# Optimization experiments

Measured on AMD Instinct MI355X. Metric: run time of the kernel, lower is better.

Reference implementation:

```python
import jax, jax.numpy as jnp
import numpy as np

N_NODES = 50000
N_EDGES = 800000
IN_FEATS = 256
H_FEATS = 256
NUM_CLASSES = 16
NUM_GRAPHS = 64


def _glorot(key, shape):
    lim = float(np.sqrt(6.0 / (shape[0] + shape[1])))
    return jax.random.uniform(key, shape, jnp.float32, -lim, lim)


def setup_inputs() -> dict:
    key = jax.random.key(0)
    ks = jax.random.split(key, 12)
    x = jax.random.normal(ks[0], (N_NODES, IN_FEATS), jnp.float32)
    edge_index = jax.random.randint(ks[1], (2, N_EDGES), 0, N_NODES, jnp.int64)
    batch_vec = jnp.sort(jax.random.randint(ks[2], (N_NODES,), 0, NUM_GRAPHS, jnp.int64))
    W1 = _glorot(ks[3], (IN_FEATS, H_FEATS)); b1 = jnp.zeros((H_FEATS,), jnp.float32)
    W2 = _glorot(ks[4], (H_FEATS, H_FEATS)); b2 = jnp.zeros((H_FEATS,), jnp.float32)
    W3 = _glorot(ks[5], (H_FEATS, H_FEATS)); b3 = jnp.zeros((H_FEATS,), jnp.float32)
    W4 = _glorot(ks[6], (H_FEATS, NUM_CLASSES)); b4 = jnp.zeros((NUM_CLASSES,), jnp.float32)
    return {"x": x, "edge_index": edge_index, "batch_vec": batch_vec,
            "W1": W1, "b1": b1, "W2": W2, "b2": b2,
            "W3": W3, "b3": b3, "W4": W4, "b4": b4}


def gcn_conv(x, W, b, src, dst, deg_inv_sqrt):
    # PyG GCNConv: out = D^{-1/2} (A + I) D^{-1/2} (x W) + b
    h = x @ W  # [N, F_out]
    norm = deg_inv_sqrt[src] * deg_inv_sqrt[dst]  # [E+N]
    msgs = h[src] * norm[:, None]  # gather + scale
    agg = jax.ops.segment_sum(msgs, dst, num_segments=x.shape[0])
    return agg + b


def reference(x, edge_index, batch_vec, W1, b1, W2, b2, W3, b3, W4, b4):
    n = x.shape[0]
    # add self-loops once (shared across layers)
    loops = jnp.arange(n, dtype=edge_index.dtype)
    src = jnp.concatenate([edge_index[0], loops])
    dst = jnp.concatenate([edge_index[1], loops])
    deg = jax.ops.segment_sum(jnp.ones_like(dst, dtype=x.dtype), dst, num_segments=n)
    deg_inv_sqrt = jnp.where(deg > 0, jax.lax.rsqrt(deg), 0.0)

    h = gcn_conv(x, W1, b1, src, dst, deg_inv_sqrt)
    h_copy = jax.nn.relu(h)
    # dropout is identity in eval mode (training=False)
    h = gcn_conv(h_copy, W2, b2, src, dst, deg_inv_sqrt)
    h_copy = jax.nn.relu(jax.nn.relu(h) + h_copy)
    h = gcn_conv(h_copy, W3, b3, src, dst, deg_inv_sqrt)
    h = jax.nn.relu(jax.nn.relu(h) + h_copy)
    h = gcn_conv(h, W4, b4, src, dst, deg_inv_sqrt)

    # global_mean_pool over batch vector
    sums = jax.ops.segment_sum(h, batch_vec, num_segments=NUM_GRAPHS)
    counts = jax.ops.segment_sum(jnp.ones((n,), h.dtype), batch_vec, num_segments=NUM_GRAPHS)
    return sums / jnp.maximum(counts, 1.0)[:, None]
```

## Files before the change

### kernel.cpp

```cpp
#include <hip/hip_runtime.h>
#include <hip/hip_bf16.h>

#define N_NODES 50000
#define N_EDGES 800000
#define F 256
#define NGRAPH 64
#define NCLS 16
#define NBLK_N 196

typedef short short8 __attribute__((ext_vector_type(8)));
typedef float f32x4 __attribute__((ext_vector_type(4)));

__device__ __forceinline__ float bf2f(ushort u) {
    unsigned v = ((unsigned)u) << 16;
    return __uint_as_float(v);
}
__device__ __forceinline__ ushort f2bf(float f) {
    __hip_bfloat16 b = __float2bfloat16(f);
    return *reinterpret_cast<ushort*>(&b);
}
__device__ __forceinline__ float bflo(uint u) { return __uint_as_float(u << 16); }
__device__ __forceinline__ float bfhi(uint u) { return __uint_as_float(u & 0xffff0000u); }


__global__ __launch_bounds__(256) void k_init(int* __restrict__ ecnt,
                                              float* __restrict__ pool,
                                              float* __restrict__ cnt) {
    int i = blockIdx.x * 256 + threadIdx.x;
    if (i < N_NODES) ecnt[i] = 0;
    if (i < NGRAPH * NCLS) pool[i] = 0.f;
    if (i < NGRAPH) cnt[i] = 0.f;
}

__global__ __launch_bounds__(256) void k_count(const int* __restrict__ dst,
                                               int* __restrict__ ecnt) {
    int e = blockIdx.x * 256 + threadIdx.x;
    if (e < N_EDGES) atomicAdd(&ecnt[dst[e]], 1);
}

__global__ __launch_bounds__(256) void k_scan_block(const int* __restrict__ ecnt,
                                                    int* __restrict__ rowptr,
                                                    int* __restrict__ blkSum,
                                                    float* __restrict__ dinv,
                                                    float* __restrict__ sdeg) {
    __shared__ int sh[256];
    int i = blockIdx.x * 256 + threadIdx.x;
    int v = (i < N_NODES) ? ecnt[i] : 0;
    sh[threadIdx.x] = v;
    __syncthreads();
#pragma unroll
    for (int off = 1; off < 256; off <<= 1) {
        int t = (threadIdx.x >= off) ? sh[threadIdx.x - off] : 0;
        __syncthreads();
        sh[threadIdx.x] += t;
        __syncthreads();
    }
    if (i < N_NODES) {
        rowptr[i] = sh[threadIdx.x] - v;
        float d = (float)(v + 1);
        dinv[i] = rsqrtf(d);
        sdeg[i] = sqrtf(d);
    }
    if (threadIdx.x == 255) blkSum[blockIdx.x] = sh[255];
}

__global__ __launch_bounds__(256) void k_scan_add(const int* __restrict__ blkSum,
                                                  int* __restrict__ rowptr,
                                                  int* __restrict__ cursor) {
    __shared__ int sh[256];
    int t = threadIdx.x;
    sh[t] = (t < NBLK_N && t < (int)blockIdx.x) ? blkSum[t] : 0;
    __syncthreads();
#pragma unroll
    for (int off = 128; off > 0; off >>= 1) {
        if (t < off) sh[t] += sh[t + off];
        __syncthreads();
    }
    int base = sh[0];
    int i = blockIdx.x * 256 + t;
    if (i < N_NODES) {
        int r = rowptr[i] + base;
        rowptr[i] = r;
        cursor[i] = r;
    }
    if (i == 0) rowptr[N_NODES] = N_EDGES;
}

__global__ __launch_bounds__(256) void k_fill_csr(const int* __restrict__ src,
                                                  const int* __restrict__ dst,
                                                  int* __restrict__ cursor,
                                                  ushort* __restrict__ csr16) {
    int e = blockIdx.x * 256 + threadIdx.x;
    if (e >= N_EDGES) return;
    int s = src[e];
    int d = dst[e];
    int p = atomicAdd(&cursor[d], 1);
    csr16[p] = (ushort)s;
}


__global__ __launch_bounds__(256) void k_prescale(const float* __restrict__ x,
                                                  const float* __restrict__ dinv,
                                                  ushort* __restrict__ T0) {
    int i = blockIdx.x * 256 + threadIdx.x;
    if (i >= (int)((size_t)N_NODES * F / 8)) return;
    int n = i >> 5;
    float di = dinv[n];
    const float4* ip = (const float4*)(x + (size_t)i * 8);
    float4 a = ip[0], b = ip[1];
    short8 v;
    v[0] = (short)f2bf(a.x * di); v[1] = (short)f2bf(a.y * di);
    v[2] = (short)f2bf(a.z * di); v[3] = (short)f2bf(a.w * di);
    v[4] = (short)f2bf(b.x * di); v[5] = (short)f2bf(b.y * di);
    v[6] = (short)f2bf(b.z * di); v[7] = (short)f2bf(b.w * di);
    *(short8*)(T0 + (size_t)i * 8) = v;
}


__global__ __launch_bounds__(256) void k_wpack(const float* __restrict__ W1,
                                               const float* __restrict__ W2,
                                               const float* __restrict__ W3,
                                               const float* __restrict__ W4,
                                               ushort* __restrict__ Wp,
                                               ushort* __restrict__ Wp4) {
    int gid = blockIdx.x * 256 + threadIdx.x;
    if (gid < 24576) {
        int which = gid >> 13;
        int idx = gid & 8191;
        const float* W = (which == 0) ? W1 : (which == 1) ? W2 : W3;
        ushort* o = Wp + (size_t)which * 65536;
        int lane = idx & 63;
        int ks = (idx >> 6) & 7;
        int ctg = idx >> 9;
        int kbase = ks * 32 + (lane >> 4) * 8;
        int col = ctg * 16 + (lane & 15);
        short8 v;
#pragma unroll
        for (int e = 0; e < 8; ++e)
            v[e] = (short)f2bf(W[(size_t)(kbase + e) * 256 + col]);
        *(short8*)(o + (size_t)idx * 8) = v;
    } else if (gid < 24576 + 512) {
        int idx = gid - 24576;
        int lane = idx & 63;
        int ks = idx >> 6;
        int kbase = ks * 32 + (lane >> 4) * 8;
        int col = lane & 15;
        short8 v;
#pragma unroll
        for (int e = 0; e < 8; ++e)
            v[e] = (short)f2bf(W4[(size_t)(kbase + e) * 16 + col]);
        *(short8*)(Wp4 + (size_t)idx * 8) = v;
    }
}


template <int MODE>
__global__ __launch_bounds__(256) void k_layer(const ushort* __restrict__ Hs,
                                               const ushort* __restrict__ Wp,
                                               const float* __restrict__ bias,
                                               const float* __restrict__ dinv,
                                               const float* __restrict__ sdeg,
                                               const int* __restrict__ rowptr,
                                               const ushort* __restrict__ csr16,
                                               ushort* __restrict__ OUT,
                                               const ushort* __restrict__ Wp4,
                                               ushort* __restrict__ G16) {
    __shared__ __align__(16) ushort At[16 * 264];
    __shared__ __align__(16) ushort cs[4][16 * 72];
    const int t = threadIdx.x;
    const int wv = t >> 6;
    const int l = t & 63;
    const int m0 = blockIdx.x * 16;

    {
        const int slot = l >> 5;
        const int c = (l & 31) * 8;
#pragma unroll
        for (int rep = 0; rep < 4; ++rep) {
            const int noderow = wv * 4 + rep;
            const int n = m0 + noderow;
            const bool valid = n < N_NODES;
            const int nn = valid ? n : 0;

            float acc[8];
#pragma unroll
            for (int j = 0; j < 8; ++j) acc[j] = 0.f;

            int i = valid ? rowptr[nn] + slot : 0;
            const int end = valid ? rowptr[nn + 1] : 0;
            for (; i + 6 < end; i += 8) {
                int s0 = csr16[i], s1 = csr16[i + 2], s2 = csr16[i + 4], s3 = csr16[i + 6];
                short8 v0 = *(const short8*)(Hs + (size_t)s0 * F + c);
                short8 v1 = *(const short8*)(Hs + (size_t)s1 * F + c);
                short8 v2 = *(const short8*)(Hs + (size_t)s2 * F + c);
                short8 v3 = *(const short8*)(Hs + (size_t)s3 * F + c);
#pragma unroll
                for (int j = 0; j < 8; ++j)
                    acc[j] += (bf2f((ushort)v0[j]) + bf2f((ushort)v1[j])) +
                              (bf2f((ushort)v2[j]) + bf2f((ushort)v3[j]));
            }
            for (; i < end; i += 2) {
                int s0 = csr16[i];
                short8 v0 = *(const short8*)(Hs + (size_t)s0 * F + c);
#pragma unroll
                for (int j = 0; j < 8; ++j) acc[j] += bf2f((ushort)v0[j]);
            }

#pragma unroll
            for (int j = 0; j < 8; ++j) acc[j] += __shfl_xor(acc[j], 32);

            if (slot == 0) {
                short8 av;
                if (valid) {
                    const short8 h = *(const short8*)(Hs + (size_t)nn * F + c);
                    float di = dinv[nn];
#pragma unroll
                    for (int j = 0; j < 8; ++j)
                        av[j] = (short)f2bf(di * (acc[j] + bf2f((ushort)h[j])));
                } else {
#pragma unroll
                    for (int j = 0; j < 8; ++j) av[j] = 0;
                }
                *(short8*)&At[noderow * 264 + c] = av;
            }
        }
    }
    __syncthreads();

    const int colbase = wv * 64;
    const int lrow = l & 15;
    const int lk = (l >> 4) * 8;
    const short8* wp = (const short8*)Wp;

    short8 af[8];
#pragma unroll
    for (int ks = 0; ks < 8; ++ks)
        af[ks] = *(const short8*)&At[lrow * 264 + lk + ks * 32];

#pragma unroll
    for (int ct = 0; ct < 4; ++ct) {
        short8 wf[8];
#pragma unroll
        for (int ks = 0; ks < 8; ++ks)
            wf[ks] = wp[(size_t)(((wv * 4 + ct) * 8 + ks) * 64) + l];

        f32x4 acc = (f32x4){0.f, 0.f, 0.f, 0.f};
#pragma unroll
        for (int ks = 0; ks < 8; ++ks)
            acc = __builtin_amdgcn_mfma_f32_16x16x32_bf16(af[ks], wf[ks], acc, 0, 0, 0);

        int col = ct * 16 + (l & 15);
#pragma unroll
        for (int r = 0; r < 4; ++r) {
            int row = (l >> 4) * 4 + r;
            cs[wv][row * 72 + col] = f2bf(acc[r]);
        }
    }
#pragma unroll
    for (int h = 0; h < 2; ++h) {
        int row = h * 8 + (l >> 3);
        int coff = (l & 7) * 8;
        int orow = m0 + row;
        if (orow < N_NODES) {
            short8 z8 = *(const short8*)&cs[wv][row * 72 + coff];
            int gcol = colbase + coff;
            const float4 b0 = *(const float4*)(bias + gcol);
            const float4 b1 = *(const float4*)(bias + gcol + 4);
            float bb[8] = {b0.x, b0.y, b0.z, b0.w, b1.x, b1.y, b1.z, b1.w};
            float di = dinv[orow];
            short8 ov;
            if (MODE >= 2) {
                const short8 hp = *(const short8*)(Hs + (size_t)orow * F + gcol);
                float sd = sdeg[orow];
#pragma unroll
                for (int j = 0; j < 8; ++j) {
                    float u = fmaxf(bf2f((ushort)z8[j]) + bb[j], 0.f);
                    u = fmaxf(u + bf2f((ushort)hp[j]) * sd, 0.f);
                    ov[j] = (short)f2bf(u * di);
                }
            } else {
#pragma unroll
                for (int j = 0; j < 8; ++j) {
                    float u = fmaxf(bf2f((ushort)z8[j]) + bb[j], 0.f);
                    ov[j] = (short)f2bf(u * di);
                }
            }
            if (MODE == 3) {
                *(short8*)&cs[wv][row * 72 + coff] = ov;
            } else {
                *(short8*)(OUT + (size_t)orow * F + gcol) = ov;
            }
        } else if (MODE == 3) {
            short8 zv;
#pragma unroll
            for (int j = 0; j < 8; ++j) zv[j] = 0;
            *(short8*)&cs[wv][row * 72 + coff] = zv;
        }
    }

    if (MODE == 3) {
        __syncthreads();
        if (wv == 0) {
            const short8* wp4 = (const short8*)Wp4;
            f32x4 acc = (f32x4){0.f, 0.f, 0.f, 0.f};
#pragma unroll
            for (int ks = 0; ks < 8; ++ks) {
                int cbase = lk + ks * 32;
                short8 a2 = *(const short8*)&cs[cbase >> 6][lrow * 72 + (cbase & 63)];
                short8 w4 = wp4[(size_t)(ks * 64) + l];
                acc = __builtin_amdgcn_mfma_f32_16x16x32_bf16(a2, w4, acc, 0, 0, 0);
            }
            int col = l & 15;
#pragma unroll
            for (int r = 0; r < 4; ++r) {
                int row = (l >> 4) * 4 + r;
                int orow = m0 + row;
                if (orow < N_NODES)
                    G16[(size_t)orow * 16 + col] = f2bf(acc[r]);
            }
        }
    }
}


__global__ __launch_bounds__(256) void k_g16pool(const ushort* __restrict__ G16,
                                                 const float* __restrict__ bias,
                                                 const float* __restrict__ dinv,
                                                 const int* __restrict__ rowptr,
                                                 const ushort* __restrict__ csr16,
                                                 const int* __restrict__ batch,
                                                 float* __restrict__ pool,
                                                 float* __restrict__ cnt) {
    __shared__ float ps[NGRAPH][NCLS];
    __shared__ float pc[NGRAPH];
    for (int i = threadIdx.x; i < NGRAPH * NCLS; i += 256) ((float*)ps)[i] = 0.f;
    if (threadIdx.x < NGRAPH) pc[threadIdx.x] = 0.f;
    __syncthreads();

    int gid = blockIdx.x * 256 + threadIdx.x;
    int n = gid >> 2;
    int q = (gid & 3) * 4;
    if (n < N_NODES) {
        float ax = 0.f, ay = 0.f, az = 0.f, aw = 0.f;
        const int end = rowptr[n + 1];
        for (int i = rowptr[n]; i < end; ++i) {
            int s0 = csr16[i];
            const uint2 u = *(const uint2*)(G16 + (size_t)s0 * 16 + q);
            ax += bflo(u.x); ay += bfhi(u.x);
            az += bflo(u.y); aw += bfhi(u.y);
        }
        const uint2 hu = *(const uint2*)(G16 + (size_t)n * 16 + q);
        const float4 b = *(const float4*)(bias + q);
        float di = dinv[n];
        int g = batch[n];
        atomicAdd(&ps[g][q + 0], b.x + di * (ax + bflo(hu.x)));
        atomicAdd(&ps[g][q + 1], b.y + di * (ay + bfhi(hu.x)));
        atomicAdd(&ps[g][q + 2], b.z + di * (az + bflo(hu.y)));
        atomicAdd(&ps[g][q + 3], b.w + di * (aw + bfhi(hu.y)));
        if ((gid & 3) == 0) atomicAdd(&pc[g], 1.f);
    }
    __syncthreads();

    for (int i = threadIdx.x; i < NGRAPH * NCLS; i += 256) {
        float v = ((float*)ps)[i];
        if (v != 0.f) unsafeAtomicAdd(&pool[i], v);
    }
    if (threadIdx.x < NGRAPH) {
        float v = pc[threadIdx.x];
        if (v > 0.f) unsafeAtomicAdd(&cnt[threadIdx.x], v);
    }
}

__global__ __launch_bounds__(256) void k_final(const float* __restrict__ pool,
                                               const float* __restrict__ cnt,
                                               float* __restrict__ out) {
    int i = blockIdx.x * 256 + threadIdx.x;
    if (i < NGRAPH * NCLS) out[i] = pool[i] / fmaxf(cnt[i >> 4], 1.f);
}


extern "C" void kernel_launch(void* const* d_in, const int* in_sizes, int n_in,
                              void* d_out, int out_size, void* d_ws, size_t ws_size,
                              hipStream_t stream) {
    const float* x   = (const float*)d_in[0];
    const int*   ei  = (const int*)d_in[1];
    const int*   bvec= (const int*)d_in[2];
    const float* W1  = (const float*)d_in[3];
    const float* b1  = (const float*)d_in[4];
    const float* W2  = (const float*)d_in[5];
    const float* b2  = (const float*)d_in[6];
    const float* W3  = (const float*)d_in[7];
    const float* b3  = (const float*)d_in[8];
    const float* W4  = (const float*)d_in[9];
    const float* b4  = (const float*)d_in[10];
    float* out = (float*)d_out;

    const int* src = ei;
    const int* dst = ei + N_EDGES;

    const size_t NF = (size_t)N_NODES * F;
    ushort* T0  = (ushort*)d_ws;
    ushort* T1  = T0 + NF;
    ushort* T2  = T1 + NF;
    ushort* G16 = T2 + NF;
    float*  aux = (float*)(G16 + (size_t)N_NODES * 16 + 64);
    int*    ecnt   = (int*)aux;
    float*  dinv   = aux + N_NODES;
    float*  sdeg   = aux + 2 * N_NODES;
    int*    rowptr = (int*)(aux + 3 * N_NODES);
    int*    cursor = (int*)(aux + 4 * N_NODES + 64);
    int*    blkSum = (int*)(aux + 5 * N_NODES + 64);
    ushort* csr16  = (ushort*)(blkSum + 256);
    float*  pool   = (float*)(csr16 + N_EDGES);
    float*  cnt    = pool + NGRAPH * NCLS;
    ushort* Wp     = (ushort*)(cnt + NGRAPH);
    ushort* Wp4    = Wp + 3 * 65536;

    const int BN = NBLK_N;
    const int BE = (N_EDGES + 255) / 256;
    const int BL = (N_NODES + 15) / 16;
    const int B4 = (N_NODES * 4 + 255) / 256;
    const int BP = (int)((NF / 8 + 255) / 256);

    k_init<<<BN, 256, 0, stream>>>(ecnt, pool, cnt);
    k_count<<<BE, 256, 0, stream>>>(dst, ecnt);
    k_scan_block<<<BN, 256, 0, stream>>>(ecnt, rowptr, blkSum, dinv, sdeg);
    k_scan_add<<<BN, 256, 0, stream>>>(blkSum, rowptr, cursor);
    k_fill_csr<<<BE, 256, 0, stream>>>(src, dst, cursor, csr16);

    k_wpack<<<99, 256, 0, stream>>>(W1, W2, W3, W4, Wp, Wp4);
    k_prescale<<<BP, 256, 0, stream>>>(x, dinv, T0);

    k_layer<1><<<BL, 256, 0, stream>>>(T0, Wp,          b1, dinv, sdeg, rowptr, csr16, T1, nullptr, nullptr);
    k_layer<2><<<BL, 256, 0, stream>>>(T1, Wp + 65536,  b2, dinv, sdeg, rowptr, csr16, T2, nullptr, nullptr);
    k_layer<3><<<BL, 256, 0, stream>>>(T2, Wp + 131072, b3, dinv, sdeg, rowptr, csr16, nullptr, Wp4, G16);

    k_g16pool<<<B4, 256, 0, stream>>>(G16, b4, dinv, rowptr, csr16, bvec, pool, cnt);

    k_final<<<4, 256, 0, stream>>>(pool, cnt, out);
}
```

Baseline: 353.6 us.

## Sort nodes by in-degree so each layer block processes degree-balanced rows

Builds a degree histogram and a counting-sort permutation of nodes, descending by in-degree, then has each layer block gather and compute its 16 rows through that permutation. The goal is to group nodes of similar degree together, so the waves in a block finish their gather loops at about the same time and heavy blocks launch first. This adds three small preprocessing kernels and scatters output rows non-contiguously. It also drops the tail bounds checks, relying on N_NODES being a multiple of 16 (50000 is). In MODE 3 the tail-zeroing of cs is removed as well.

Measured after the change: 628.2 us. 77.7% more time.

```diff
diff --git a/kernel.cpp b/kernel.cpp
--- a/kernel.cpp
+++ b/kernel.cpp
@@ -25,17 +25,51 @@
 
 __global__ __launch_bounds__(256) void k_init(int* __restrict__ ecnt,
                                               float* __restrict__ pool,
-                                              float* __restrict__ cnt) {
+                                              float* __restrict__ cnt,
+                                              int* __restrict__ hist) {
     int i = blockIdx.x * 256 + threadIdx.x;
     if (i < N_NODES) ecnt[i] = 0;
     if (i < NGRAPH * NCLS) pool[i] = 0.f;
     if (i < NGRAPH) cnt[i] = 0.f;
+    if (i < 256) hist[i] = 0;
 }
 
 __global__ __launch_bounds__(256) void k_count(const int* __restrict__ dst,
                                                int* __restrict__ ecnt) {
     int e = blockIdx.x * 256 + threadIdx.x;
     if (e < N_EDGES) atomicAdd(&ecnt[dst[e]], 1);
+}
+
+__global__ __launch_bounds__(256) void k_hist(const int* __restrict__ ecnt,
+                                              int* __restrict__ hist) {
+    int i = blockIdx.x * 256 + threadIdx.x;
+    if (i < N_NODES) atomicAdd(&hist[min(ecnt[i], 255)], 1);
+}
+
+__global__ __launch_bounds__(256) void k_offs(const int* __restrict__ hist,
+                                              int* __restrict__ offs) {
+    __shared__ int sh[256];
+    int t = threadIdx.x;
+    sh[t] = hist[t];
+    __syncthreads();
+    if (t == 0) {
+        int run = 0;
+        for (int b = 255; b >= 0; --b) { int h = sh[b]; sh[b] = run; run += h; }
+    }
+    __syncthreads();
+    offs[t] = sh[t];
+    offs[256 + t] = sh[t];
+}
+
+__global__ __launch_bounds__(256) void k_permfill(const int* __restrict__ ecnt,
+                                                  int* __restrict__ pcur,
+                                                  int* __restrict__ perm) {
+    int i = blockIdx.x * 256 + threadIdx.x;
+    if (i < N_NODES) {
+        int b = min(ecnt[i], 255);
+        int p = atomicAdd(&pcur[b], 1);
+        perm[p] = i;
+    }
 }
 
 __global__ __launch_bounds__(256) void k_scan_block(const int* __restrict__ ecnt,
@@ -162,32 +196,35 @@
                                                const float* __restrict__ sdeg,
                                                const int* __restrict__ rowptr,
                                                const ushort* __restrict__ csr16,
+                                               const int* __restrict__ perm,
                                                ushort* __restrict__ OUT,
                                                const ushort* __restrict__ Wp4,
                                                ushort* __restrict__ G16) {
     __shared__ __align__(16) ushort At[16 * 264];
     __shared__ __align__(16) ushort cs[4][16 * 72];
+    __shared__ int pn[16];
     const int t = threadIdx.x;
     const int wv = t >> 6;
     const int l = t & 63;
     const int m0 = blockIdx.x * 16;
 
+    if (t < 16) pn[t] = perm[m0 + t];
+    __syncthreads();
+
     {
         const int slot = l >> 5;
         const int c = (l & 31) * 8;
 #pragma unroll
         for (int rep = 0; rep < 4; ++rep) {
             const int noderow = wv * 4 + rep;
-            const int n = m0 + noderow;
-            const bool valid = n < N_NODES;
-            const int nn = valid ? n : 0;
+            const int nn = pn[noderow];
 
             float acc[8];
 #pragma unroll
             for (int j = 0; j < 8; ++j) acc[j] = 0.f;
 
-            int i = valid ? rowptr[nn] + slot : 0;
-            const int end = valid ? rowptr[nn + 1] : 0;
+            int i = rowptr[nn] + slot;
+            const int end = rowptr[nn + 1];
             for (; i + 6 < end; i += 8) {
                 int s0 = csr16[i], s1 = csr16[i + 2], s2 = csr16[i + 4], s3 = csr16[i + 6];
                 short8 v0 = *(const short8*)(Hs + (size_t)s0 * F + c);
@@ -210,17 +247,12 @@
             for (int j = 0; j < 8; ++j) acc[j] += __shfl_xor(acc[j], 32);
 
             if (slot == 0) {
+                const short8 h = *(const short8*)(Hs + (size_t)nn * F + c);
+                float di = dinv[nn];
                 short8 av;
-                if (valid) {
-                    const short8 h = *(const short8*)(Hs + (size_t)nn * F + c);
-                    float di = dinv[nn];
-#pragma unroll
-                    for (int j = 0; j < 8; ++j)
-                        av[j] = (short)f2bf(di * (acc[j] + bf2f((ushort)h[j])));
-                } else {
-#pragma unroll
-                    for (int j = 0; j < 8; ++j) av[j] = 0;
-                }
+#pragma unroll
+                for (int j = 0; j < 8; ++j)
+                    av[j] = (short)f2bf(di * (acc[j] + bf2f((ushort)h[j])));
                 *(short8*)&At[noderow * 264 + c] = av;
             }
         }
@@ -260,8 +292,8 @@
     for (int h = 0; h < 2; ++h) {
         int row = h * 8 + (l >> 3);
         int coff = (l & 7) * 8;
-        int orow = m0 + row;
-        if (orow < N_NODES) {
+        int orow = pn[row];
+        {
             short8 z8 = *(const short8*)&cs[wv][row * 72 + coff];
             int gcol = colbase + coff;
             const float4 b0 = *(const float4*)(bias + gcol);
@@ -290,11 +322,6 @@
             } else {
                 *(short8*)(OUT + (size_t)orow * F + gcol) = ov;
             }
-        } else if (MODE == 3) {
-            short8 zv;
-#pragma unroll
-            for (int j = 0; j < 8; ++j) zv[j] = 0;
-            *(short8*)&cs[wv][row * 72 + coff] = zv;
         }
     }
 
@@ -314,9 +341,8 @@
 #pragma unroll
             for (int r = 0; r < 4; ++r) {
                 int row = (l >> 4) * 4 + r;
-                int orow = m0 + row;
-                if (orow < N_NODES)
-                    G16[(size_t)orow * 16 + col] = f2bf(acc[r]);
+                int orow = pn[row];
+                G16[(size_t)orow * 16 + col] = f2bf(acc[r]);
             }
         }
     }
@@ -409,8 +435,11 @@
     float*  sdeg   = aux + 2 * N_NODES;
     int*    rowptr = (int*)(aux + 3 * N_NODES);
     int*    cursor = (int*)(aux + 4 * N_NODES + 64);
-    int*    blkSum = (int*)(aux + 5 * N_NODES + 64);
-    ushort* csr16  = (ushort*)(blkSum + 256);
+    int*    perm   = (int*)(aux + 5 * N_NODES + 64);
+    int*    blkSum = (int*)(aux + 6 * N_NODES + 64);
+    int*    hist   = blkSum + 256;
+    int*    offs   = hist + 256;
+    ushort* csr16  = (ushort*)(offs + 512);
     float*  pool   = (float*)(csr16 + N_EDGES);
     float*  cnt    = pool + NGRAPH * NCLS;
     ushort* Wp     = (ushort*)(cnt + NGRAPH);
@@ -422,8 +451,11 @@
     const int B4 = (N_NODES * 4 + 255) / 256;
     const int BP = (int)((NF / 8 + 255) / 256);
 
-    k_init<<<BN, 256, 0, stream>>>(ecnt, pool, cnt);
+    k_init<<<BN, 256, 0, stream>>>(ecnt, pool, cnt, hist);
     k_count<<<BE, 256, 0, stream>>>(dst, ecnt);
+    k_hist<<<BN, 256, 0, stream>>>(ecnt, hist);
+    k_offs<<<1, 256, 0, stream>>>(hist, offs);
+    k_permfill<<<BN, 256, 0, stream>>>(ecnt, offs + 256, perm);
     k_scan_block<<<BN, 256, 0, stream>>>(ecnt, rowptr, blkSum, dinv, sdeg);
     k_scan_add<<<BN, 256, 0, stream>>>(blkSum, rowptr, cursor);
     k_fill_csr<<<BE, 256, 0, stream>>>(src, dst, cursor, csr16);
@@ -431,9 +463,9 @@
     k_wpack<<<99, 256, 0, stream>>>(W1, W2, W3, W4, Wp, Wp4);
     k_prescale<<<BP, 256, 0, stream>>>(x, dinv, T0);
 
-    k_layer<1><<<BL, 256, 0, stream>>>(T0, Wp,          b1, dinv, sdeg, rowptr, csr16, T1, nullptr, nullptr);
-    k_layer<2><<<BL, 256, 0, stream>>>(T1, Wp + 65536,  b2, dinv, sdeg, rowptr, csr16, T2, nullptr, nullptr);
-    k_layer<3><<<BL, 256, 0, stream>>>(T2, Wp + 131072, b3, dinv, sdeg, rowptr, csr16, nullptr, Wp4, G16);
+    k_layer<1><<<BL, 256, 0, stream>>>(T0, Wp,          b1, dinv, sdeg, rowptr, csr16, perm, T1, nullptr, nullptr);
+    k_layer<2><<<BL, 256, 0, stream>>>(T1, Wp + 65536,  b2, dinv, sdeg, rowptr, csr16, perm, T2, nullptr, nullptr);
+    k_layer<3><<<BL, 256, 0, stream>>>(T2, Wp + 131072, b3, dinv, sdeg, rowptr, csr16, perm, nullptr, Wp4, G16);
 
     k_g16pool<<<B4, 256, 0, stream>>>(G16, b4, dinv, rowptr, csr16, bvec, pool, cnt);
 
```
